# Kernel optimization log

Hardware: AMD Instinct MI355X
Metric: run time of the kernel (lower is better)

## Reference

```python
import jax, jax.numpy as jnp
import numpy as np

S = 0.7071067811865476  # 1/sqrt(2), haar filter coefficient


def wavelet_kernels():
    # pywt haar: dec_lo=[s,s], dec_hi=[-s,s], rec_lo=[s,s], rec_hi=[s,-s]
    # module reverses dec filters -> dec_lo_rev=[s,s], dec_hi_rev=[s,-s]
    lo_d = jnp.array([S, S], jnp.float32)
    hi_d = jnp.array([S, -S], jnp.float32)
    lo_r = jnp.array([S, S], jnp.float32)
    hi_r = jnp.array([S, -S], jnp.float32)
    # torch builds k[i,j] = row_filter[i] * col_filter[j] with (row, col) = (2nd, 1st) unsqueeze
    Kd = jnp.stack([jnp.outer(lo_d, lo_d), jnp.outer(hi_d, lo_d),
                    jnp.outer(lo_d, hi_d), jnp.outer(hi_d, hi_d)])  # [4,2,2] LL,LH,HL,HH
    Kr = 4.0 * jnp.stack([jnp.outer(lo_r, lo_r), jnp.outer(hi_r, lo_r),
                          jnp.outer(lo_r, hi_r), jnp.outer(hi_r, hi_r)])  # rec_* * 4
    return Kd, Kr


def group_norm(x, gamma, beta, groups, eps=1e-5):
    B, C, H, W = x.shape
    xg = x.reshape(B, groups, C // groups, H, W)
    mu = xg.mean(axis=(2, 3, 4), keepdims=True)
    var = xg.var(axis=(2, 3, 4), keepdims=True)
    xn = ((xg - mu) * jax.lax.rsqrt(var + eps)).reshape(B, C, H, W)
    return xn * gamma[None, :, None, None] + beta[None, :, None, None]


def conv2d(x, w, b, stride=1, pad=1):
    y = jax.lax.conv_general_dilated(x, w, (stride, stride), [(pad, pad), (pad, pad)],
                                     dimension_numbers=('NCHW', 'OIHW', 'NCHW'))
    return y + b[None, :, None, None]


def conv_transpose2d(x, w, b, stride=2, pad=1):
    # w in torch layout [Cin, Cout, kh, kw]; transpose conv == conv with
    # lhs-dilated input, spatially flipped kernel, padding k-1-pad
    wf = jnp.flip(w, (-2, -1)).transpose(1, 0, 2, 3)
    p = w.shape[-1] - 1 - pad
    y = jax.lax.conv_general_dilated(x, wf, (1, 1), [(p, p), (p, p)],
                                     lhs_dilation=(stride, stride),
                                     dimension_numbers=('NCHW', 'OIHW', 'NCHW'))
    return y + b[None, :, None, None]


def dwt2d(x, Kd):
    # haar k=2, stride=2, pad=0 -> non-overlapping 2x2 blocks; exact conv2d equivalent
    B, C, H, W = x.shape
    xr = x.reshape(B, C, H // 2, 2, W // 2, 2)
    c = jnp.einsum('bchdwe,sde->bcshw', xr, Kd)  # s in {LL,LH,HL,HH}
    return c.reshape(B, C * 4, H // 2, W // 2)   # channel layout [c0:LL,LH,HL,HH, c1:...]


def idwt2d(c, Kr):
    # conv_transpose2d k=2, stride=2, pad=0 -> pure 2x2 interleave
    B, C4, Hh, Wh = c.shape
    C = C4 // 4
    cr = c.reshape(B, C, 4, Hh, Wh)
    y = jnp.einsum('bcshw,sde->bchdwe', cr, Kr)
    return y.reshape(B, C, 2 * Hh, 2 * Wh)


def _forward(x, Kd, Kr, W1, b1, g1, be1, W2, b2, g2, be2, W3, b3, g3, be3,
             W4, b4, g4, be4, Wt, bt, g5, be5, W6, b6):
    h = dwt2d(x, Kd)                                      # [B,32,H/2,W/2]
    h = jax.nn.relu(group_norm(conv2d(h, W1, b1, 1, 1), g1, be1, 8))    # 32->64
    h = jax.nn.relu(group_norm(conv2d(h, W2, b2, 2, 1), g2, be2, 16))   # 64->128, /2
    h = jax.nn.relu(group_norm(conv2d(h, W3, b3, 1, 1), g3, be3, 32))   # 128->256
    h = jax.nn.relu(group_norm(conv2d(h, W4, b4, 1, 1), g4, be4, 16))   # 256->128
    h = jax.nn.relu(group_norm(conv_transpose2d(h, Wt, bt, 2, 1), g5, be5, 8))  # 128->64, x2
    h = conv2d(h, W6, b6, 1, 1)                            # 64->16
    return idwt2d(h, Kr)                                   # [B,4,H,W]


def setup_inputs() -> dict:
    key = jax.random.key(0)
    ks = jax.random.split(key, 16)
    B, Cin, H, W = 16, 8, 256, 256
    bc = 64
    Kd, Kr = wavelet_kernels()
    w = lambda k, s: jax.random.normal(k, s, jnp.float32) * 0.05
    return {
        'x': jax.random.normal(ks[0], (B, Cin, H, W), jnp.float32),
        'Kd': Kd, 'Kr': Kr,
        'W1': w(ks[1], (bc, Cin * 4, 3, 3)), 'b1': jnp.zeros(bc),
        'g1': jnp.ones(bc), 'be1': jnp.zeros(bc),
        'W2': w(ks[2], (bc * 2, bc, 3, 3)), 'b2': jnp.zeros(bc * 2),
        'g2': jnp.ones(bc * 2), 'be2': jnp.zeros(bc * 2),
        'W3': w(ks[3], (bc * 4, bc * 2, 3, 3)), 'b3': jnp.zeros(bc * 4),
        'g3': jnp.ones(bc * 4), 'be3': jnp.zeros(bc * 4),
        'W4': w(ks[4], (bc * 2, bc * 4, 3, 3)), 'b4': jnp.zeros(bc * 2),
        'g4': jnp.ones(bc * 2), 'be4': jnp.zeros(bc * 2),
        'Wt': w(ks[5], (bc * 2, bc, 4, 4)), 'bt': jnp.zeros(bc),  # torch convT layout [in,out,kh,kw]
        'g5': jnp.ones(bc), 'be5': jnp.zeros(bc),
        'W6': w(ks[6], (4 * 4, bc, 3, 3)), 'b6': jnp.zeros(4 * 4),
    }


def reference(x, Kd, Kr, W1, b1, g1, be1, W2, b2, g2, be2, W3, b3, g3, be3,
              W4, b4, g4, be4, Wt, bt, g5, be5, W6, b6):
    return _forward(x, Kd, Kr, W1, b1, g1, be1, W2, b2, g2, be2, W3, b3, g3, be3,
                    W4, b4, g4, be4, Wt, bt, g5, be5, W6, b6)
```

## Files before the change

### kernel.cpp

```cpp
#include <hip/hip_runtime.h>

typedef unsigned short ushort_t;
typedef unsigned int uint_t;
typedef __attribute__((ext_vector_type(8))) short short8;
typedef __attribute__((ext_vector_type(4))) float f32x4;

#define PAD 40

__device__ __forceinline__ ushort_t f2bf(float f) {
    uint_t u = __float_as_uint(f);
    u = (u + 0x7FFFu + ((u >> 16) & 1u)) >> 16;
    return (ushort_t)u;
}
__device__ __forceinline__ float bf2f(ushort_t h) {
    return __uint_as_float(((uint_t)h) << 16);
}

__device__ __forceinline__ void red_stats(float& s, float& ss) {
    s += __shfl_xor(s, 16); ss += __shfl_xor(ss, 16);
    s += __shfl_xor(s, 32); ss += __shfl_xor(ss, 32);
    s += __shfl_xor(s, 1);  ss += __shfl_xor(ss, 1);
    s += __shfl_xor(s, 2);  ss += __shfl_xor(ss, 2);
    s += __shfl_xor(s, 4);  ss += __shfl_xor(ss, 4);
}

__device__ __forceinline__ uint4 gn8(uint4 v, const float2* ss) {
    uint_t u[4] = {v.x, v.y, v.z, v.w};
    uint_t r[4];
#pragma unroll
    for (int p = 0; p < 4; ++p) {
        float2 s0 = ss[2 * p], s1 = ss[2 * p + 1];
        float f0 = fmaxf(bf2f((ushort_t)(u[p] & 0xffffu)) * s0.x + s0.y, 0.f);
        float f1 = fmaxf(bf2f((ushort_t)(u[p] >> 16)) * s1.x + s1.y, 0.f);
        r[p] = (uint_t)f2bf(f0) | ((uint_t)f2bf(f1) << 16);
    }
    return make_uint4(r[0], r[1], r[2], r[3]);
}

template<int C, int NPB>
__device__ __forceinline__ void fill_ss(float2* sshare, const float2* __restrict__ pin,
                                        const float* __restrict__ gamma,
                                        const float* __restrict__ beta,
                                        int b, float invC, int tid) {
    for (int c = tid; c < C; c += 256) {
        const float2* p = pin + ((size_t)b * (C / 8) + (c >> 3)) * NPB;
        float s = 0.f, ss = 0.f;
#pragma unroll 8
        for (int i = 0; i < NPB; ++i) { s += p[i].x; ss += p[i].y; }
        float mean = s * invC;
        float rstd = rsqrtf(ss * invC - mean * mean + 1e-5f);
        float sc = gamma[c] * rstd;
        sshare[c] = make_float2(sc, beta[c] - mean * sc);
    }
}

template<int CIN, int COUT>
__device__ __forceinline__ void pack3(const float* __restrict__ W, ushort_t* __restrict__ wp, int idx) {
    int kk = idx & 31;
    int t = idx >> 5;
    int co = t % COUT; t /= COUT;
    int tap = t % 9;
    int cib = t / 9;
    wp[idx] = f2bf(W[(co * CIN + cib * 32 + kk) * 9 + tap]);
}

__device__ __forceinline__ void pack2p(const float* __restrict__ W2, ushort_t* __restrict__ wp, int idx) {
    int kk = idx & 31;
    int co = (idx >> 5) & 127;
    int tap = (idx >> 12) & 3;
    int cib = idx >> 14;
    int p = cib >> 2, q = (cib >> 1) & 1, chalf = cib & 1;
    int kh = 2 * (tap >> 1) + p - 1;
    int kw = 2 * (tap & 1) + q - 1;
    float v = 0.f;
    if (kh >= 0 && kh < 3 && kw >= 0 && kw < 3)
        v = W2[(co * 64 + chalf * 32 + kk) * 9 + kh * 3 + kw];
    wp[idx] = f2bf(v);
}

__device__ __forceinline__ void packt(const float* __restrict__ Wt, ushort_t* __restrict__ wp, int idx) {
    int kk = idx & 31;
    int t = idx >> 5;
    int co = t & 63; t >>= 6;
    int tap = t & 3; t >>= 2;
    int cib = t & 3;
    int ph = t >> 2;
    int rs = tap >> 1, cs = tap & 1;
    int eh = ph >> 1, ew = ph & 1;
    int kh = eh ? (rs ? 0 : 2) : (rs ? 1 : 3);
    int kw = ew ? (cs ? 0 : 2) : (cs ? 1 : 3);
    wp[idx] = f2bf(Wt[((cib * 32 + kk) * 64 + co) * 16 + kh * 4 + kw]);
}

__global__ __launch_bounds__(256) void pack_all(const float* __restrict__ W1,
                                                const float* __restrict__ W2,
                                                const float* __restrict__ W3,
                                                const float* __restrict__ W4,
                                                const float* __restrict__ Wt,
                                                const float* __restrict__ W6,
                                                ushort_t* __restrict__ WP) {
    int idx = blockIdx.x * 256 + threadIdx.x;
    if (idx < 18432)        pack3<32, 64>(W1, WP, idx);
    else if (idx < 149504)  pack2p(W2, WP + 18432, idx - 18432);
    else if (idx < 444416)  pack3<128, 256>(W3, WP + 149504, idx - 149504);
    else if (idx < 739328)  pack3<256, 128>(W4, WP + 444416, idx - 444416);
    else if (idx < 870400)  packt(Wt, WP + 739328, idx - 739328);
    else if (idx < 879616)  pack3<64, 16>(W6, WP + 870400, idx - 870400);
}

__global__ __launch_bounds__(256) void dwt_nhwc(const float* __restrict__ x,
                                                const float* __restrict__ Kd,
                                                ushort_t* __restrict__ out) {
    int idx = blockIdx.x * 256 + threadIdx.x;
    int w = idx & 127, h = (idx >> 7) & 127, b = idx >> 14;
    float k[16];
#pragma unroll
    for (int i = 0; i < 16; ++i) k[i] = Kd[i];
    const float* xb = x + (size_t)b * 8 * 65536;
    uint_t uu[16];
#pragma unroll
    for (int ci = 0; ci < 8; ++ci) {
        const float* p = xb + ci * 65536 + (2 * h) * 256 + 2 * w;
        float2 r0 = *(const float2*)p;
        float2 r1 = *(const float2*)(p + 256);
        ushort_t o[4];
#pragma unroll
        for (int sb = 0; sb < 4; ++sb) {
            float v = r0.x * k[sb*4] + r0.y * k[sb*4+1] + r1.x * k[sb*4+2] + r1.y * k[sb*4+3];
            o[sb] = f2bf(v);
        }
        uu[ci*2]   = (uint_t)o[0] | ((uint_t)o[1] << 16);
        uu[ci*2+1] = (uint_t)o[2] | ((uint_t)o[3] << 16);
    }
    uint4* dst = (uint4*)(out + (size_t)idx * 32);
    dst[0] = make_uint4(uu[0], uu[1], uu[2], uu[3]);
    dst[1] = make_uint4(uu[4], uu[5], uu[6], uu[7]);
    dst[2] = make_uint4(uu[8], uu[9], uu[10], uu[11]);
    dst[3] = make_uint4(uu[12], uu[13], uu[14], uu[15]);
}

__global__ __launch_bounds__(256) void idwt_nhwc(const ushort_t* __restrict__ cin,
                                                 const float* __restrict__ Kr,
                                                 float* __restrict__ out) {
    int idx = blockIdx.x * 256 + threadIdx.x;
    int w = idx & 127, h = (idx >> 7) & 127, b = idx >> 14;
    float k[16];
#pragma unroll
    for (int i = 0; i < 16; ++i) k[i] = Kr[i];
    const uint4* pv = (const uint4*)(cin + (size_t)idx * 16);
    uint4 v0 = pv[0], v1 = pv[1];
    uint_t uw[8] = {v0.x, v0.y, v0.z, v0.w, v1.x, v1.y, v1.z, v1.w};
    float cs[16];
#pragma unroll
    for (int i = 0; i < 8; ++i) {
        cs[2*i]   = bf2f((ushort_t)(uw[i] & 0xffffu));
        cs[2*i+1] = bf2f((ushort_t)(uw[i] >> 16));
    }
#pragma unroll
    for (int c = 0; c < 4; ++c) {
        float y00 = 0, y01 = 0, y10 = 0, y11 = 0;
#pragma unroll
        for (int sb = 0; sb < 4; ++sb) {
            float v = cs[c * 4 + sb];
            y00 += v * k[sb*4];   y01 += v * k[sb*4+1];
            y10 += v * k[sb*4+2]; y11 += v * k[sb*4+3];
        }
        float* ob = out + ((size_t)(b * 4 + c) * 256 + 2 * h) * 256 + 2 * w;
        *(float2*)ob = make_float2(y00, y01);
        *(float2*)(ob + 256) = make_float2(y10, y11);
    }
}

template<int CIN, int COUT, int H, int W, bool STATS, bool GNIN, int NPBI>
__global__ __launch_bounds__(256, 2) void conv_mfma(const ushort_t* __restrict__ in,
                                                    const ushort_t* __restrict__ wp,
                                                    const float* __restrict__ bias,
                                                    ushort_t* __restrict__ outp,
                                                    float2* __restrict__ pstats_out,
                                                    const float2* __restrict__ pstats_in,
                                                    const float* __restrict__ gamma,
                                                    const float* __restrict__ beta,
                                                    float invC) {
    constexpr int NT = (COUT < 64) ? COUT : 64;
    constexpr int NF = NT / 16;
    constexpr int NCB = CIN / 32;
    constexpr int CSTR = (CIN < 64) ? CIN : 64;
    constexpr int NBI = CIN / CSTR;
    constexpr int SUB = CSTR / 32;
    constexpr int NBO = COUT / NT;
    constexpr int IW = 66, NRI = 6;
    constexpr int AITER = NRI * IW * 4;
    constexpr int CA = (AITER + 255) / 256;
    constexpr int BITER = 9 * NT * 4;
    constexpr int CB = (BITER + 255) / 256;
    constexpr int NW = W / 64, NH = H / 4;
    constexpr int PB = NBO * NW * NH;
    constexpr int NPBO = NH * NW;
    constexpr int EP = NT + 8;

    __shared__ ushort_t smem[NRI * IW * PAD + 9 * NT * PAD];
    __shared__ float2 sred[4][8];
    __shared__ float2 sshare[CIN];
    ushort_t* lA = smem;
    ushort_t* lB = smem + NRI * IW * PAD;
    ushort_t* lE = smem;

    int bid = blockIdx.x;
    int xcd = bid & 7;
    int rest = bid >> 3;
    int half = rest / PB;
    int local = rest - half * PB;
    int b = xcd + 8 * half;
    int ht = local % NH; local /= NH;
    int wt = local % NW; local /= NW;
    int nb = local;
    int h0 = ht * 4, w0 = wt * 64, n0 = nb * NT;
    int tid = threadIdx.x;
    int lane = tid & 63, wid = tid >> 6;
    int nl = lane & 15, quad = lane >> 4, ql = quad * 8;

    if (GNIN) {
        fill_ss<CIN, NPBI>(sshare, pstats_in, gamma, beta, b, invC, tid);
        __syncthreads();
    }

    int ga[CA], la[CA], pr[CA];
#pragma unroll
    for (int r = 0; r < CA; ++r) {
        int i = tid + r * 256;
        ga[r] = -1; la[r] = 0; pr[r] = 0;
        if (i < AITER) {
            int tr = i / (IW * 4); int rem = i - tr * (IW * 4);
            int p = rem >> 2, part = rem & 3;
            la[r] = (tr * IW + p) * PAD + part * 8;
            pr[r] = part;
            int ih = h0 - 1 + tr, iw = w0 - 1 + p;
            if ((unsigned)ih < (unsigned)H && (unsigned)iw < (unsigned)W)
                ga[r] = (ih * W + iw) * CSTR + part * 8;
        }
    }
    int gb[CB], lb[CB];
#pragma unroll
    for (int r = 0; r < CB; ++r) {
        int i = tid + r * 256;
        gb[r] = -1; lb[r] = 0;
        if (i < BITER) {
            int tap = i / (NT * 4); int rem = i - tap * (NT * 4);
            int co = rem >> 2, part = rem & 3;
            gb[r] = (tap * COUT + n0 + co) * 32 + part * 8;
            lb[r] = (tap * NT + co) * PAD + part * 8;
        }
    }

    f32x4 acc[4][NF];
#pragma unroll
    for (int mf = 0; mf < 4; ++mf)
#pragma unroll
        for (int nf = 0; nf < NF; ++nf)
            acc[mf][nf] = (f32x4){0.f, 0.f, 0.f, 0.f};

    uint4 ra[CA], rb[CB];

    auto loadA = [&](int cib) {
        const int blk = cib / SUB;
        const int inner = (cib - blk * SUB) * 32;
        const ushort_t* base = in + ((size_t)(b * NBI + blk) * (H * W)) * CSTR + inner;
#pragma unroll
        for (int r = 0; r < CA; ++r) {
            uint4 v = make_uint4(0, 0, 0, 0);
            if (ga[r] >= 0) {
                v = *(const uint4*)(base + ga[r]);
                if (GNIN) v = gn8(v, &sshare[cib * 32 + pr[r] * 8]);
            }
            ra[r] = v;
        }
    };
    auto loadB = [&](int cib) {
        const ushort_t* wb = wp + (size_t)cib * 9 * COUT * 32;
#pragma unroll
        for (int r = 0; r < CB; ++r)
            if (gb[r] >= 0) rb[r] = *(const uint4*)(wb + gb[r]);
    };

    loadA(0); loadB(0);

    for (int cib = 0; cib < NCB; ++cib) {
        __syncthreads();
#pragma unroll
        for (int r = 0; r < CA; ++r)
            if (tid + r * 256 < AITER) *(uint4*)&lA[la[r]] = ra[r];
#pragma unroll
        for (int r = 0; r < CB; ++r)
            if (tid + r * 256 < BITER) *(uint4*)&lB[lb[r]] = rb[r];
        __syncthreads();
        if (cib + 1 < NCB) { loadA(cib + 1); loadB(cib + 1); }

#pragma unroll
        for (int tap = 0; tap < 9; ++tap) {
            const int kh = tap / 3, kw = tap % 3;
            short8 af[4];
#pragma unroll
            for (int mf = 0; mf < 4; ++mf)
                af[mf] = *(const short8*)&lA[((wid + kh) * IW + mf * 16 + nl + kw) * PAD + ql];
            short8 bf[NF];
#pragma unroll
            for (int nf = 0; nf < NF; ++nf)
                bf[nf] = *(const short8*)&lB[(tap * NT + nf * 16 + nl) * PAD + ql];
#pragma unroll
            for (int mf = 0; mf < 4; ++mf)
#pragma unroll
                for (int nf = 0; nf < NF; ++nf)
                    acc[mf][nf] = __builtin_amdgcn_mfma_f32_16x16x32_bf16(
                        af[mf], bf[nf], acc[mf][nf], 0, 0, 0);
        }
    }

    float bs[NF];
#pragma unroll
    for (int nf = 0; nf < NF; ++nf) bs[nf] = bias[n0 + nf * 16 + nl];

    if (STATS) {
#pragma unroll
        for (int nf = 0; nf < NF; ++nf) {
            float s = 0.f, ss = 0.f;
#pragma unroll
            for (int mf = 0; mf < 4; ++mf)
#pragma unroll
                for (int rg = 0; rg < 4; ++rg) {
                    float v = acc[mf][nf][rg] + bs[nf];
                    s += v; ss += v * v;
                }
            red_stats(s, ss);
            if (quad == 0 && (nl & 7) == 0) sred[wid][nf * 2 + (nl >> 3)] = make_float2(s, ss);
        }
    }

    __syncthreads();
#pragma unroll
    for (int mf = 0; mf < 4; ++mf)
#pragma unroll
        for (int nf = 0; nf < NF; ++nf)
#pragma unroll
            for (int rg = 0; rg < 4; ++rg) {
                int px = wid * 64 + mf * 16 + quad * 4 + rg;
                lE[px * EP + nf * 16 + nl] = f2bf(acc[mf][nf][rg] + bs[nf]);
            }
    __syncthreads();
#pragma unroll
    for (int it = 0; it < NT / 8; ++it) {
        int idx = it * 256 + tid;
        int px = idx / (NT / 8), ck = idx % (NT / 8);
        int row = px >> 6, col = px & 63;
        uint4 v = *(const uint4*)&lE[px * EP + ck * 8];
        *(uint4*)(outp + ((((size_t)(b * NBO + nb) * H + h0 + row) * W + w0 + col) * NT + ck * 8)) = v;
    }
    if (STATS && tid < 2 * NF) {
        float2 t0 = sred[0][tid], t1 = sred[1][tid], t2 = sred[2][tid], t3 = sred[3][tid];
        pstats_out[((size_t)b * (COUT / 8) + (n0 >> 3) + tid) * NPBO + (ht * NW + wt)] =
            make_float2(t0.x + t1.x + t2.x + t3.x, t0.y + t1.y + t2.y + t3.y);
    }
}

__global__ __launch_bounds__(256, 2) void conv2p_mfma(const ushort_t* __restrict__ in,
                                                      const ushort_t* __restrict__ wp,
                                                      const float* __restrict__ bias,
                                                      ushort_t* __restrict__ outp,
                                                      float2* __restrict__ pstats_out,
                                                      const float2* __restrict__ pstats_in,
                                                      const float* __restrict__ gamma,
                                                      const float* __restrict__ beta,
                                                      float invC) {
    constexpr int IW = 65, NRI = 5, NF = 4, NT = 64;
    constexpr int AITER = NRI * IW * 4;
    constexpr int CA = 6, CB = 4;
    constexpr int EP = NT + 8;
    __shared__ ushort_t smem[NRI * IW * PAD + 4 * NT * PAD];
    __shared__ float2 sred[4][8];
    __shared__ float2 sshare[64];
    ushort_t* lA = smem;
    ushort_t* lB = smem + NRI * IW * PAD;
    ushort_t* lE = smem;

    int bid = blockIdx.x;
    int xcd = bid & 7;
    int rest = bid >> 3;
    int half = rest >> 5;
    int local = rest & 31;
    int b = xcd + 8 * half;
    int ht = local & 15;
    int nb = local >> 4;
    int h0 = ht * 4, n0 = nb * 64;
    int tid = threadIdx.x;
    int lane = tid & 63, wid = tid >> 6;
    int nl = lane & 15, quad = lane >> 4, ql = quad * 8;

    fill_ss<64, 64>(sshare, pstats_in, gamma, beta, b, invC, tid);
    __syncthreads();

    int r2[CA], c2[CA], la[CA], g4[CA], pr[CA];
#pragma unroll
    for (int r = 0; r < CA; ++r) {
        int i = tid + r * 256;
        r2[r] = -1000; c2[r] = 0; la[r] = 0; g4[r] = 0; pr[r] = 0;
        if (i < AITER) {
            int tr = i / (IW * 4); int rem = i - tr * (IW * 4);
            int p = rem >> 2, part = rem & 3;
            r2[r] = 2 * (h0 - 1 + tr);
            c2[r] = 2 * (p - 1);
            la[r] = (tr * IW + p) * PAD + part * 8;
            g4[r] = part * 8;
            pr[r] = part;
        }
    }
    int gb[CB], lb[CB];
#pragma unroll
    for (int r = 0; r < CB; ++r) {
        int i = tid + r * 256;
        int tap = i >> 8, co = (i >> 2) & 63, part = i & 3;
        gb[r] = (tap * 128 + n0 + co) * 32 + part * 8;
        lb[r] = (tap * NT + co) * PAD + part * 8;
    }

    f32x4 acc[4][NF];
#pragma unroll
    for (int mf = 0; mf < 4; ++mf)
#pragma unroll
        for (int nf = 0; nf < NF; ++nf)
            acc[mf][nf] = (f32x4){0.f, 0.f, 0.f, 0.f};

    const ushort_t* ibase = in + (size_t)b * 128 * 128 * 64;
    uint4 ra[CA], rb[CB];

    auto loadA = [&](int cib) {
        const int p = cib >> 2, q = (cib >> 1) & 1, ch32 = (cib & 1) * 32;
#pragma unroll
        for (int r = 0; r < CA; ++r) {
            int ih = r2[r] + p, iw = c2[r] + q;
            uint4 v = make_uint4(0, 0, 0, 0);
            if ((unsigned)ih < 128u && (unsigned)iw < 128u) {
                v = *(const uint4*)(ibase + ((ih << 7) + iw) * 64 + ch32 + g4[r]);
                v = gn8(v, &sshare[ch32 + pr[r] * 8]);
            }
            ra[r] = v;
        }
    };
    auto loadB = [&](int cib) {
        const ushort_t* wb = wp + (size_t)cib * 4 * 128 * 32;
#pragma unroll
        for (int r = 0; r < CB; ++r)
            rb[r] = *(const uint4*)(wb + gb[r]);
    };

    loadA(0); loadB(0);

#pragma unroll
    for (int cib = 0; cib < 8; ++cib) {
        const int p = cib >> 2, q = (cib >> 1) & 1;
        __syncthreads();
#pragma unroll
        for (int r = 0; r < CA; ++r)
            if (tid + r * 256 < AITER) *(uint4*)&lA[la[r]] = ra[r];
#pragma unroll
        for (int r = 0; r < CB; ++r) *(uint4*)&lB[lb[r]] = rb[r];
        __syncthreads();
        if (cib + 1 < 8) { loadA(cib + 1); loadB(cib + 1); }

#pragma unroll
        for (int kh = 0; kh < 2; ++kh)
#pragma unroll
            for (int kw = 0; kw < 2; ++kw)
                if ((kh == 1 || p == 1) && (kw == 1 || q == 1)) {
                    short8 af[4];
#pragma unroll
                    for (int mf = 0; mf < 4; ++mf)
                        af[mf] = *(const short8*)&lA[((wid + kh) * IW + mf * 16 + nl + kw) * PAD + ql];
                    short8 bf[NF];
#pragma unroll
                    for (int nf = 0; nf < NF; ++nf)
                        bf[nf] = *(const short8*)&lB[((kh * 2 + kw) * NT + nf * 16 + nl) * PAD + ql];
#pragma unroll
                    for (int mf = 0; mf < 4; ++mf)
#pragma unroll
                        for (int nf = 0; nf < NF; ++nf)
                            acc[mf][nf] = __builtin_amdgcn_mfma_f32_16x16x32_bf16(
                                af[mf], bf[nf], acc[mf][nf], 0, 0, 0);
                }
    }

    float bs[NF];
#pragma unroll
    for (int nf = 0; nf < NF; ++nf) bs[nf] = bias[n0 + nf * 16 + nl];
#pragma unroll
    for (int nf = 0; nf < NF; ++nf) {
        float s = 0.f, ss = 0.f;
#pragma unroll
        for (int mf = 0; mf < 4; ++mf)
#pragma unroll
            for (int rg = 0; rg < 4; ++rg) {
                float v = acc[mf][nf][rg] + bs[nf];
                s += v; ss += v * v;
            }
        red_stats(s, ss);
        if (quad == 0 && (nl & 7) == 0) sred[wid][nf * 2 + (nl >> 3)] = make_float2(s, ss);
    }

    __syncthreads();
#pragma unroll
    for (int mf = 0; mf < 4; ++mf)
#pragma unroll
        for (int nf = 0; nf < NF; ++nf)
#pragma unroll
            for (int rg = 0; rg < 4; ++rg) {
                int px = wid * 64 + mf * 16 + quad * 4 + rg;
                lE[px * EP + nf * 16 + nl] = f2bf(acc[mf][nf][rg] + bs[nf]);
            }
    __syncthreads();
#pragma unroll
    for (int it = 0; it < 8; ++it) {
        int idx = it * 256 + tid;
        int px = idx >> 3, ck = idx & 7;
        int row = px >> 6, col = px & 63;
        uint4 v = *(const uint4*)&lE[px * EP + ck * 8];
        *(uint4*)(outp + ((((size_t)(b * 2 + nb) * 64 + h0 + row) * 64 + col) * 64 + ck * 8)) = v;
    }
    if (tid < 8) {
        float2 t0 = sred[0][tid], t1 = sred[1][tid], t2 = sred[2][tid], t3 = sred[3][tid];
        pstats_out[((size_t)b * 16 + (n0 >> 3) + tid) * 16 + ht] =
            make_float2(t0.x + t1.x + t2.x + t3.x, t0.y + t1.y + t2.y + t3.y);
    }
}

__global__ __launch_bounds__(256, 2) void convt_mfma(const ushort_t* __restrict__ in,
                                                     const ushort_t* __restrict__ wp,
                                                     const float* __restrict__ bias,
                                                     ushort_t* __restrict__ outp,
                                                     float2* __restrict__ pstats_out,
                                                     const float2* __restrict__ pstats_in,
                                                     const float* __restrict__ gamma,
                                                     const float* __restrict__ beta,
                                                     float invC) {
    constexpr int CIN = 128, COUT = 64, NT = 64, NF = 4;
    constexpr int IW = 66, NRI = 5;
    constexpr int AITER = NRI * IW * 4;
    constexpr int CA = 6, CB = 4;
    constexpr int EP = NT + 8;
    __shared__ ushort_t smem[NRI * IW * PAD + 4 * NT * PAD];
    __shared__ float2 sred[4][8];
    __shared__ float2 sshare[CIN];
    ushort_t* lA = smem;
    ushort_t* lB = smem + NRI * IW * PAD;
    ushort_t* lE = smem;

    int bid = blockIdx.x;
    int xcd = bid & 7;
    int rest = bid >> 3;
    int half = rest >> 6;
    int local = rest & 63;
    int b = xcd + 8 * half;
    int ht = local & 15;
    int ph = local >> 4;
    int eh = ph >> 1, ew = ph & 1;
    int ho0 = ht * 4;
    int tid = threadIdx.x;
    int lane = tid & 63, wid = tid >> 6;
    int nl = lane & 15, quad = lane >> 4, ql = quad * 8;

    fill_ss<CIN, 16>(sshare, pstats_in, gamma, beta, b, invC, tid);
    __syncthreads();

    int ga[CA], la[CA], pr[CA];
#pragma unroll
    for (int r = 0; r < CA; ++r) {
        int i = tid + r * 256;
        ga[r] = -1; la[r] = 0; pr[r] = 0;
        if (i < AITER) {
            int tr = i / (IW * 4); int rem = i - tr * (IW * 4);
            int p = rem >> 2, part = rem & 3;
            la[r] = (tr * IW + p) * PAD + part * 8;
            pr[r] = part;
            int ih = ho0 + tr - (1 - eh), iw = p - 1;
            if ((unsigned)ih < 64u && (unsigned)iw < 64u)
                ga[r] = (ih * 64 + iw) * 64 + part * 8;
        }
    }
    int gb[CB], lb[CB];
#pragma unroll
    for (int r = 0; r < CB; ++r) {
        int i = tid + r * 256;
        int tap = i >> 8, co = (i >> 2) & 63, part = i & 3;
        gb[r] = (tap * COUT + co) * 32 + part * 8;
        lb[r] = (tap * NT + co) * PAD + part * 8;
    }

    f32x4 acc[4][NF];
#pragma unroll
    for (int mf = 0; mf < 4; ++mf)
#pragma unroll
        for (int nf = 0; nf < NF; ++nf)
            acc[mf][nf] = (f32x4){0.f, 0.f, 0.f, 0.f};

    uint4 ra[CA], rb[CB];

    auto loadA = [&](int cib) {
        const int blk = cib >> 1;
        const int inner = (cib & 1) * 32;
        const ushort_t* base = in + ((size_t)(b * 2 + blk) * 4096) * 64 + inner;
#pragma unroll
        for (int r = 0; r < CA; ++r) {
            uint4 v = make_uint4(0, 0, 0, 0);
            if (ga[r] >= 0) {
                v = *(const uint4*)(base + ga[r]);
                v = gn8(v, &sshare[cib * 32 + pr[r] * 8]);
            }
            ra[r] = v;
        }
    };
    auto loadB = [&](int cib) {
        const ushort_t* wb = wp + ((size_t)ph * 4 + cib) * 4 * COUT * 32;
#pragma unroll
        for (int r = 0; r < CB; ++r)
            rb[r] = *(const uint4*)(wb + gb[r]);
    };

    loadA(0); loadB(0);

    for (int cib = 0; cib < 4; ++cib) {
        __syncthreads();
#pragma unroll
        for (int r = 0; r < CA; ++r)
            if (tid + r * 256 < AITER) *(uint4*)&lA[la[r]] = ra[r];
#pragma unroll
        for (int r = 0; r < CB; ++r) *(uint4*)&lB[lb[r]] = rb[r];
        __syncthreads();
        if (cib + 1 < 4) { loadA(cib + 1); loadB(cib + 1); }

#pragma unroll
        for (int tap = 0; tap < 4; ++tap) {
            const int rs = tap >> 1, cs = tap & 1;
            short8 af[4];
#pragma unroll
            for (int mf = 0; mf < 4; ++mf)
                af[mf] = *(const short8*)&lA[((wid + rs) * IW + mf * 16 + nl + cs + ew) * PAD + ql];
            short8 bf[NF];
#pragma unroll
            for (int nf = 0; nf < NF; ++nf)
                bf[nf] = *(const short8*)&lB[(tap * NT + nf * 16 + nl) * PAD + ql];
#pragma unroll
            for (int mf = 0; mf < 4; ++mf)
#pragma unroll
                for (int nf = 0; nf < NF; ++nf)
                    acc[mf][nf] = __builtin_amdgcn_mfma_f32_16x16x32_bf16(
                        af[mf], bf[nf], acc[mf][nf], 0, 0, 0);
        }
    }

    float bs[NF];
#pragma unroll
    for (int nf = 0; nf < NF; ++nf) bs[nf] = bias[nf * 16 + nl];
#pragma unroll
    for (int nf = 0; nf < NF; ++nf) {
        float s = 0.f, ss = 0.f;
#pragma unroll
        for (int mf = 0; mf < 4; ++mf)
#pragma unroll
            for (int rg = 0; rg < 4; ++rg) {
                float v = acc[mf][nf][rg] + bs[nf];
                s += v; ss += v * v;
            }
        red_stats(s, ss);
        if (quad == 0 && (nl & 7) == 0) sred[wid][nf * 2 + (nl >> 3)] = make_float2(s, ss);
    }

    __syncthreads();
#pragma unroll
    for (int mf = 0; mf < 4; ++mf)
#pragma unroll
        for (int nf = 0; nf < NF; ++nf)
#pragma unroll
            for (int rg = 0; rg < 4; ++rg) {
                int px = wid * 64 + mf * 16 + quad * 4 + rg;
                lE[px * EP + nf * 16 + nl] = f2bf(acc[mf][nf][rg] + bs[nf]);
            }
    __syncthreads();
#pragma unroll
    for (int it = 0; it < 8; ++it) {
        int idx = it * 256 + tid;
        int px = idx >> 3, ck = idx & 7;
        int row = px >> 6, wo = px & 63;
        int oh = 2 * (ho0 + row) + eh;
        uint4 v = *(const uint4*)&lE[px * EP + ck * 8];
        *(uint4*)(outp + (((size_t)b * 128 + oh) * 128 + 2 * wo + ew) * 64 + ck * 8) = v;
    }
    if (tid < 8) {
        float2 t0 = sred[0][tid], t1 = sred[1][tid], t2 = sred[2][tid], t3 = sred[3][tid];
        pstats_out[((size_t)b * 8 + tid) * 64 + (ht * 4 + ph)] =
            make_float2(t0.x + t1.x + t2.x + t3.x, t0.y + t1.y + t2.y + t3.y);
    }
}

extern "C" void kernel_launch(void* const* d_in, const int* in_sizes, int n_in,
                              void* d_out, int out_size, void* d_ws, size_t ws_size,
                              hipStream_t stream) {
    const float* x   = (const float*)d_in[0];
    const float* Kd  = (const float*)d_in[1];
    const float* Kr  = (const float*)d_in[2];
    const float* W1  = (const float*)d_in[3];  const float* b1  = (const float*)d_in[4];
    const float* g1  = (const float*)d_in[5];  const float* be1 = (const float*)d_in[6];
    const float* W2  = (const float*)d_in[7];  const float* b2  = (const float*)d_in[8];
    const float* g2  = (const float*)d_in[9];  const float* be2 = (const float*)d_in[10];
    const float* W3  = (const float*)d_in[11]; const float* b3  = (const float*)d_in[12];
    const float* g3  = (const float*)d_in[13]; const float* be3 = (const float*)d_in[14];
    const float* W4  = (const float*)d_in[15]; const float* b4  = (const float*)d_in[16];
    const float* g4  = (const float*)d_in[17]; const float* be4 = (const float*)d_in[18];
    const float* Wt  = (const float*)d_in[19]; const float* bt  = (const float*)d_in[20];
    const float* g5  = (const float*)d_in[21]; const float* be5 = (const float*)d_in[22];
    const float* W6  = (const float*)d_in[23]; const float* b6  = (const float*)d_in[24];

    ushort_t* U  = (ushort_t*)d_ws;
    ushort_t* V  = U + 8388608;
    ushort_t* WP = V + 16777216;
    ushort_t* wp1 = WP;
    ushort_t* wp2 = WP + 18432;
    ushort_t* wp3 = WP + 149504;
    ushort_t* wp4 = WP + 444416;
    ushort_t* wpt = WP + 739328;
    ushort_t* wp6 = WP + 870400;
    float2* PS = (float2*)(WP + 879616);
    float2* P1 = PS;
    float2* P2 = PS + 8192;
    float2* P3 = PS + 12288;
    float2* P4 = PS + 20480;
    float2* P5 = PS + 24576;
    float* out = (float*)d_out;

    pack_all<<<3436, 256, 0, stream>>>(W1, W2, W3, W4, Wt, W6, WP);

    dwt_nhwc<<<1024, 256, 0, stream>>>(x, Kd, U);

    conv_mfma<32, 64, 128, 128, true, false, 16>
        <<<1024, 256, 0, stream>>>(U, wp1, b1, V, P1, nullptr, nullptr, nullptr, 0.f);

    conv2p_mfma<<<512, 256, 0, stream>>>(V, wp2, b2, U, P2,
                                         P1, g1, be1, 1.f / 131072.f);

    conv_mfma<128, 256, 64, 64, true, true, 16>
        <<<1024, 256, 0, stream>>>(U, wp3, b3, V, P3,
                                   P2, g2, be2, 1.f / 32768.f);

    conv_mfma<256, 128, 64, 64, true, true, 16>
        <<<512, 256, 0, stream>>>(V, wp4, b4, U, P4,
                                  P3, g3, be3, 1.f / 32768.f);

    convt_mfma<<<1024, 256, 0, stream>>>(U, wpt, bt, V, P5,
                                         P4, g4, be4, 1.f / 32768.f);

    conv_mfma<64, 16, 128, 128, false, true, 64>
        <<<1024, 256, 0, stream>>>(V, wp6, b6, U, nullptr,
                                   P5, g5, be5, 1.f / 131072.f);

    idwt_nhwc<<<1024, 256, 0, stream>>>(U, Kr, out);
}
```

Measured before the change: 448.2 us.

## Load conv weight fragments directly from global memory instead of staging in LDS

Across the three MFMA conv kernels, weight (B) tiles are no longer staged through shared memory. Each lane now reads its own short8 fragments straight from global memory, one tap ahead in a small register double buffer. This cuts LDS writes and reads, shrinks shared-memory footprint (possibly raising occupancy) and frees staging registers. The cost is many small, less coalesced global and L2 loads issued inside the MFMA loop, with latency exposed between taps.

```diff
diff --git a/kernel.cpp b/kernel.cpp
--- a/kernel.cpp
+++ b/kernel.cpp
@@ -191,18 +191,17 @@
     constexpr int IW = 66, NRI = 6;
     constexpr int AITER = NRI * IW * 4;
     constexpr int CA = (AITER + 255) / 256;
-    constexpr int BITER = 9 * NT * 4;
-    constexpr int CB = (BITER + 255) / 256;
     constexpr int NW = W / 64, NH = H / 4;
     constexpr int PB = NBO * NW * NH;
     constexpr int NPBO = NH * NW;
     constexpr int EP = NT + 8;
-
-    __shared__ ushort_t smem[NRI * IW * PAD + 9 * NT * PAD];
+    constexpr int ASZ = NRI * IW * PAD;
+    constexpr int SMEM = (ASZ > 256 * EP) ? ASZ : 256 * EP;
+
+    __shared__ ushort_t smem[SMEM];
     __shared__ float2 sred[4][8];
     __shared__ float2 sshare[CIN];
     ushort_t* lA = smem;
-    ushort_t* lB = smem + NRI * IW * PAD;
     ushort_t* lE = smem;
 
     int bid = blockIdx.x;
@@ -239,18 +238,6 @@
                 ga[r] = (ih * W + iw) * CSTR + part * 8;
         }
     }
-    int gb[CB], lb[CB];
-#pragma unroll
-    for (int r = 0; r < CB; ++r) {
-        int i = tid + r * 256;
-        gb[r] = -1; lb[r] = 0;
-        if (i < BITER) {
-            int tap = i / (NT * 4); int rem = i - tap * (NT * 4);
-            int co = rem >> 2, part = rem & 3;
-            gb[r] = (tap * COUT + n0 + co) * 32 + part * 8;
-            lb[r] = (tap * NT + co) * PAD + part * 8;
-        }
-    }
 
     f32x4 acc[4][NF];
 #pragma unroll
@@ -259,7 +246,7 @@
         for (int nf = 0; nf < NF; ++nf)
             acc[mf][nf] = (f32x4){0.f, 0.f, 0.f, 0.f};
 
-    uint4 ra[CA], rb[CB];
+    uint4 ra[CA];
 
     auto loadA = [&](int cib) {
         const int blk = cib / SUB;
@@ -275,43 +262,45 @@
             ra[r] = v;
         }
     };
-    auto loadB = [&](int cib) {
-        const ushort_t* wb = wp + (size_t)cib * 9 * COUT * 32;
-#pragma unroll
-        for (int r = 0; r < CB; ++r)
-            if (gb[r] >= 0) rb[r] = *(const uint4*)(wb + gb[r]);
-    };
-
-    loadA(0); loadB(0);
+
+    loadA(0);
+
+    const ushort_t* wlane = wp + ((size_t)(n0 + nl)) * 32 + ql;
 
     for (int cib = 0; cib < NCB; ++cib) {
         __syncthreads();
 #pragma unroll
         for (int r = 0; r < CA; ++r)
             if (tid + r * 256 < AITER) *(uint4*)&lA[la[r]] = ra[r];
-#pragma unroll
-        for (int r = 0; r < CB; ++r)
-            if (tid + r * 256 < BITER) *(uint4*)&lB[lb[r]] = rb[r];
         __syncthreads();
-        if (cib + 1 < NCB) { loadA(cib + 1); loadB(cib + 1); }
+        if (cib + 1 < NCB) loadA(cib + 1);
+
+        const ushort_t* wc = wlane + (size_t)cib * 9 * COUT * 32;
+        short8 bfc[NF], bfn[NF];
+#pragma unroll
+        for (int nf = 0; nf < NF; ++nf)
+            bfc[nf] = *(const short8*)(wc + nf * 512);
 
 #pragma unroll
         for (int tap = 0; tap < 9; ++tap) {
             const int kh = tap / 3, kw = tap % 3;
+            if (tap < 8) {
+#pragma unroll
+                for (int nf = 0; nf < NF; ++nf)
+                    bfn[nf] = *(const short8*)(wc + (size_t)(tap + 1) * COUT * 32 + nf * 512);
+            }
             short8 af[4];
 #pragma unroll
             for (int mf = 0; mf < 4; ++mf)
                 af[mf] = *(const short8*)&lA[((wid + kh) * IW + mf * 16 + nl + kw) * PAD + ql];
-            short8 bf[NF];
-#pragma unroll
-            for (int nf = 0; nf < NF; ++nf)
-                bf[nf] = *(const short8*)&lB[(tap * NT + nf * 16 + nl) * PAD + ql];
 #pragma unroll
             for (int mf = 0; mf < 4; ++mf)
 #pragma unroll
                 for (int nf = 0; nf < NF; ++nf)
                     acc[mf][nf] = __builtin_amdgcn_mfma_f32_16x16x32_bf16(
-                        af[mf], bf[nf], acc[mf][nf], 0, 0, 0);
+                        af[mf], bfc[nf], acc[mf][nf], 0, 0, 0);
+#pragma unroll
+            for (int nf = 0; nf < NF; ++nf) bfc[nf] = bfn[nf];
         }
     }
 
@@ -372,13 +361,14 @@
                                                       float invC) {
     constexpr int IW = 65, NRI = 5, NF = 4, NT = 64;
     constexpr int AITER = NRI * IW * 4;
-    constexpr int CA = 6, CB = 4;
+    constexpr int CA = 6;
     constexpr int EP = NT + 8;
-    __shared__ ushort_t smem[NRI * IW * PAD + 4 * NT * PAD];
+    constexpr int ASZ = NRI * IW * PAD;
+    constexpr int SMEM = (ASZ > 256 * EP) ? ASZ : 256 * EP;
+    __shared__ ushort_t smem[SMEM];
     __shared__ float2 sred[4][8];
     __shared__ float2 sshare[64];
     ushort_t* lA = smem;
-    ushort_t* lB = smem + NRI * IW * PAD;
     ushort_t* lE = smem;
 
     int bid = blockIdx.x;
@@ -412,14 +402,6 @@
             pr[r] = part;
         }
     }
-    int gb[CB], lb[CB];
-#pragma unroll
-    for (int r = 0; r < CB; ++r) {
-        int i = tid + r * 256;
-        int tap = i >> 8, co = (i >> 2) & 63, part = i & 3;
-        gb[r] = (tap * 128 + n0 + co) * 32 + part * 8;
-        lb[r] = (tap * NT + co) * PAD + part * 8;
-    }
 
     f32x4 acc[4][NF];
 #pragma unroll
@@ -429,7 +411,7 @@
             acc[mf][nf] = (f32x4){0.f, 0.f, 0.f, 0.f};
 
     const ushort_t* ibase = in + (size_t)b * 128 * 128 * 64;
-    uint4 ra[CA], rb[CB];
+    uint4 ra[CA];
 
     auto loadA = [&](int cib) {
         const int p = cib >> 2, q = (cib >> 1) & 1, ch32 = (cib & 1) * 32;
@@ -444,14 +426,9 @@
             ra[r] = v;
         }
     };
-    auto loadB = [&](int cib) {
-        const ushort_t* wb = wp + (size_t)cib * 4 * 128 * 32;
-#pragma unroll
-        for (int r = 0; r < CB; ++r)
-            rb[r] = *(const uint4*)(wb + gb[r]);
-    };
-
-    loadA(0); loadB(0);
+
+    loadA(0);
+    const ushort_t* wlane = wp + ((size_t)(n0 + nl)) * 32 + ql;
 
 #pragma unroll
     for (int cib = 0; cib < 8; ++cib) {
@@ -460,24 +437,24 @@
 #pragma unroll
         for (int r = 0; r < CA; ++r)
             if (tid + r * 256 < AITER) *(uint4*)&lA[la[r]] = ra[r];
-#pragma unroll
-        for (int r = 0; r < CB; ++r) *(uint4*)&lB[lb[r]] = rb[r];
         __syncthreads();
-        if (cib + 1 < 8) { loadA(cib + 1); loadB(cib + 1); }
-
+        if (cib + 1 < 8) loadA(cib + 1);
+
+        const ushort_t* wc = wlane + (size_t)cib * 4 * 128 * 32;
 #pragma unroll
         for (int kh = 0; kh < 2; ++kh)
 #pragma unroll
             for (int kw = 0; kw < 2; ++kw)
                 if ((kh == 1 || p == 1) && (kw == 1 || q == 1)) {
+                    const int tap = kh * 2 + kw;
+                    short8 bf[NF];
+#pragma unroll
+                    for (int nf = 0; nf < NF; ++nf)
+                        bf[nf] = *(const short8*)(wc + (size_t)tap * 128 * 32 + nf * 512);
                     short8 af[4];
 #pragma unroll
                     for (int mf = 0; mf < 4; ++mf)
                         af[mf] = *(const short8*)&lA[((wid + kh) * IW + mf * 16 + nl + kw) * PAD + ql];
-                    short8 bf[NF];
-#pragma unroll
-                    for (int nf = 0; nf < NF; ++nf)
-                        bf[nf] = *(const short8*)&lB[((kh * 2 + kw) * NT + nf * 16 + nl) * PAD + ql];
 #pragma unroll
                     for (int mf = 0; mf < 4; ++mf)
 #pragma unroll
@@ -542,13 +519,14 @@
     constexpr int CIN = 128, COUT = 64, NT = 64, NF = 4;
     constexpr int IW = 66, NRI = 5;
     constexpr int AITER = NRI * IW * 4;
-    constexpr int CA = 6, CB = 4;
+    constexpr int CA = 6;
     constexpr int EP = NT + 8;
-    __shared__ ushort_t smem[NRI * IW * PAD + 4 * NT * PAD];
+    constexpr int ASZ = NRI * IW * PAD;
+    constexpr int SMEM = (ASZ > 256 * EP) ? ASZ : 256 * EP;
+    __shared__ ushort_t smem[SMEM];
     __shared__ float2 sred[4][8];
     __shared__ float2 sshare[CIN];
     ushort_t* lA = smem;
-    ushort_t* lB = smem + NRI * IW * PAD;
     ushort_t* lE = smem;
 
     int bid = blockIdx.x;
@@ -583,14 +561,6 @@
                 ga[r] = (ih * 64 + iw) * 64 + part * 8;
         }
     }
-    int gb[CB], lb[CB];
-#pragma unroll
-    for (int r = 0; r < CB; ++r) {
-        int i = tid + r * 256;
-        int tap = i >> 8, co = (i >> 2) & 63, part = i & 3;
-        gb[r] = (tap * COUT + co) * 32 + part * 8;
-        lb[r] = (tap * NT + co) * PAD + part * 8;
-    }
 
     f32x4 acc[4][NF];
 #pragma unroll
@@ -599,7 +569,7 @@
         for (int nf = 0; nf < NF; ++nf)
             acc[mf][nf] = (f32x4){0.f, 0.f, 0.f, 0.f};
 
-    uint4 ra[CA], rb[CB];
+    uint4 ra[CA];
 
     auto loadA = [&](int cib) {
         const int blk = cib >> 1;
@@ -615,42 +585,44 @@
             ra[r] = v;
         }
     };
-    auto loadB = [&](int cib) {
-        const ushort_t* wb = wp + ((size_t)ph * 4 + cib) * 4 * COUT * 32;
-#pragma unroll
-        for (int r = 0; r < CB; ++r)
-            rb[r] = *(const uint4*)(wb + gb[r]);
-    };
-
-    loadA(0); loadB(0);
+
+    loadA(0);
+    const ushort_t* wlane = wp + ((size_t)ph * 4) * 4 * COUT * 32 + (size_t)nl * 32 + ql;
 
     for (int cib = 0; cib < 4; ++cib) {
         __syncthreads();
 #pragma unroll
         for (int r = 0; r < CA; ++r)
             if (tid + r * 256 < AITER) *(uint4*)&lA[la[r]] = ra[r];
-#pragma unroll
-        for (int r = 0; r < CB; ++r) *(uint4*)&lB[lb[r]] = rb[r];
         __syncthreads();
-        if (cib + 1 < 4) { loadA(cib + 1); loadB(cib + 1); }
+        if (cib + 1 < 4) loadA(cib + 1);
+
+        const ushort_t* wc = wlane + (size_t)cib * 4 * COUT * 32;
+        short8 bfc[NF], bfn[NF];
+#pragma unroll
+        for (int nf = 0; nf < NF; ++nf)
+            bfc[nf] = *(const short8*)(wc + nf * 512);
 
 #pragma unroll
         for (int tap = 0; tap < 4; ++tap) {
             const int rs = tap >> 1, cs = tap & 1;
+            if (tap < 3) {
+#pragma unroll
+                for (int nf = 0; nf < NF; ++nf)
+                    bfn[nf] = *(const short8*)(wc + (size_t)(tap + 1) * COUT * 32 + nf * 512);
+            }
             short8 af[4];
 #pragma unroll
             for (int mf = 0; mf < 4; ++mf)
                 af[mf] = *(const short8*)&lA[((wid + rs) * IW + mf * 16 + nl + cs + ew) * PAD + ql];
-            short8 bf[NF];
-#pragma unroll
-            for (int nf = 0; nf < NF; ++nf)
-                bf[nf] = *(const short8*)&lB[(tap * NT + nf * 16 + nl) * PAD + ql];
 #pragma unroll
             for (int mf = 0; mf < 4; ++mf)
 #pragma unroll
                 for (int nf = 0; nf < NF; ++nf)
                     acc[mf][nf] = __builtin_amdgcn_mfma_f32_16x16x32_bf16(
-                        af[mf], bf[nf], acc[mf][nf], 0, 0, 0);
+                        af[mf], bfc[nf], acc[mf][nf], 0, 0, 0);
+#pragma unroll
+            for (int nf = 0; nf < NF; ++nf) bfc[nf] = bfn[nf];
         }
     }
 
```

Measured after the change: 368.0 us. 1.22x faster.
